# Performance work log

Hardware: AMD Instinct MI355X
Metric: run time of the kernel (lower is better)

## Reference

```python
import jax, jax.numpy as jnp
import numpy as np

K = 8          # knn_graph default k
LOW = 64       # low_res_size
FIRE = 0.5     # fire_rate
HID = 16       # hidden_channels
HEADS = 4      # GAT heads
OUTC = HID // HEADS  # per-head out channels = 4
EPS = 1e-5


def conv3x3(x, W, b):
    y = jax.lax.conv_general_dilated(x, W, (1, 1), 'SAME',
                                     dimension_numbers=('NCHW', 'OIHW', 'NCHW'))
    return y + b[None, :, None, None]


def bnorm(x, g, b, m, v):
    scale = (g / jnp.sqrt(v + EPS))[None, :, None, None]
    return (x - m[None, :, None, None]) * scale + b[None, :, None, None]


def conv1x1(x, W, b):  # W: [out, in]
    return jnp.einsum('bchw,oc->bohw', x, W) + b[None, :, None, None]


def gat_image(nodes, Wg, a_src, a_dst, bg):
    # nodes: [N, HID]. kNN graph (loop=False) + GATConv with self-loops added.
    N = nodes.shape[0]
    sq = jnp.sum(nodes * nodes, axis=1)
    D = sq[:, None] + sq[None, :] - 2.0 * (nodes @ nodes.T)
    D = jax.lax.stop_gradient(D) + jnp.eye(N, dtype=nodes.dtype) * 1e9  # exclude self
    idx = jax.lax.top_k(-D, K)[1]                                   # [N, K] nearest nbrs
    nbr = jnp.concatenate([idx, jnp.arange(N)[:, None]], axis=1)    # [N, K+1] + self-loop
    xp = (nodes @ Wg.T).reshape(N, HEADS, OUTC)                     # [N, H, F]
    asr = jnp.sum(xp * a_src[None], axis=-1)                        # [N, H]
    adt = jnp.sum(xp * a_dst[None], axis=-1)                        # [N, H]
    logits = jax.nn.leaky_relu(asr[nbr] + adt[:, None, :], 0.2)     # [N, K+1, H]
    att = jax.nn.softmax(logits, axis=1)                            # softmax over incoming edges
    out = jnp.sum(att[..., None] * xp[nbr], axis=1)                 # [N, H, F]
    out = out.reshape(N, HEADS * OUTC) + bg
    return jax.nn.relu(out)                                         # GrapherModule relu


def setup_inputs() -> dict:
    key = jax.random.key(0)
    ks = jax.random.split(key, 24)
    f = jnp.float32
    d = {}
    d['x'] = jax.random.normal(ks[0], (8, 1, 256, 256), f)
    d['fire_rand'] = jax.random.uniform(ks[1], (8, 1, LOW, LOW), f)
    # encoder_b1: conv(1->64,3) BN conv(64->16,3) BN
    d['W1'] = jax.random.normal(ks[2], (64, 1, 3, 3), f) * 0.2
    d['b1'] = jax.random.normal(ks[3], (64,), f) * 0.05
    d['g1'] = jnp.ones((64,), f); d['be1'] = jnp.zeros((64,), f)
    d['m1'] = jax.random.normal(ks[4], (64,), f) * 0.1
    d['v1'] = jax.random.uniform(ks[5], (64,), f) + 0.5
    d['W2'] = jax.random.normal(ks[6], (HID, 64, 3, 3), f) * 0.05
    d['b2'] = jax.random.normal(ks[7], (HID,), f) * 0.05
    d['g2'] = jnp.ones((HID,), f); d['be2'] = jnp.zeros((HID,), f)
    d['m2'] = jax.random.normal(ks[8], (HID,), f) * 0.1
    d['v2'] = jax.random.uniform(ks[9], (HID,), f) + 0.5
    # GATConv(16 -> 4 per head, heads=4)
    d['Wg'] = jax.random.normal(ks[10], (HEADS * OUTC, HID), f) * 0.25
    d['a_src'] = jax.random.normal(ks[11], (HEADS, OUTC), f) * 0.5
    d['a_dst'] = jax.random.normal(ks[12], (HEADS, OUTC), f) * 0.5
    d['bg'] = jax.random.normal(ks[13], (HEADS * OUTC,), f) * 0.05
    # update_net_b1: 1x1 conv 16->128->16
    d['Wu1'] = jax.random.normal(ks[14], (128, HID), f) * 0.25
    d['bu1'] = jax.random.normal(ks[15], (128,), f) * 0.05
    d['Wu2'] = jax.random.normal(ks[16], (HID, 128), f) * 0.08
    d['bu2'] = jax.random.normal(ks[17], (HID,), f) * 0.05
    # to_output_b1: 1x1 conv 16->1
    d['Wo'] = jax.random.normal(ks[18], (1, HID), f) * 0.25
    d['bo'] = jax.random.normal(ks[19], (1,), f) * 0.05
    return d


def reference(x, fire_rand, W1, b1, g1, be1, m1, v1, W2, b2, g2, be2, m2, v2,
              Wg, a_src, a_dst, bg, Wu1, bu1, Wu2, bu2, Wo, bo):
    B, C, H, W = x.shape
    xl = jax.image.resize(x, (B, C, LOW, LOW), 'bilinear')
    h = jax.nn.relu(bnorm(conv3x3(xl, W1, b1), g1, be1, m1, v1))
    h = jax.nn.relu(bnorm(conv3x3(h, W2, b2), g2, be2, m2, v2))
    # one NCA step: graph process -> update net -> stochastic fire mask
    N = LOW * LOW
    nodes = h.reshape(B, HID, N).transpose(0, 2, 1)            # [B, N, HID]
    p = jax.vmap(gat_image, in_axes=(0, None, None, None, None))(nodes, Wg, a_src, a_dst, bg)
    p = p.transpose(0, 2, 1).reshape(B, HID, LOW, LOW)
    u = conv1x1(jax.nn.relu(conv1x1(p, Wu1, bu1)), Wu2, bu2)
    mask = (fire_rand < FIRE).astype(h.dtype)                   # [B,1,LOW,LOW]
    h = h + mask * u
    out = jax.nn.sigmoid(conv1x1(h, Wo, bo))
    return jax.image.resize(out, (B, C, H, W), 'bilinear')
```

## Files before the change

### kernel.cpp

```cpp
#include <hip/hip_runtime.h>
#include <math.h>
#include <float.h>

#define BATCH 8
#define HIGH  256
#define LOWR  64
#define NN    4096
#define HIDC  16
#define C1    64
#define NSL   4

#define OFF_XL   0
#define OFF_H1   (OFF_XL  + BATCH*NN)
#define OFF_H    (OFF_H1  + BATCH*C1*NN)
#define OFF_SQ   (OFF_H   + BATCH*NN*HIDC)
#define OFF_XP   (OFF_SQ  + BATCH*NN)
#define OFF_ASR  (OFF_XP  + BATCH*NN*HIDC)
#define OFF_ADT  (OFF_ASR + BATCH*NN*4)
#define OFF_P    (OFF_ADT + BATCH*NN*4)
#define OFF_OL   (OFF_P   + BATCH*NN*HIDC)

typedef __attribute__((ext_vector_type(8)))  short bf16x8;
typedef __attribute__((ext_vector_type(16))) float f32x16;

__device__ __forceinline__ float dot16m(const float ni[16], float4 a0, float4 a1,
                                        float4 a2, float4 a3, float hs) {
    return ni[0]*a0.x + ni[1]*a0.y + ni[2]*a0.z + ni[3]*a0.w
         + ni[4]*a1.x + ni[5]*a1.y + ni[6]*a1.z + ni[7]*a1.w
         + ni[8]*a2.x + ni[9]*a2.y + ni[10]*a2.z + ni[11]*a2.w
         + ni[12]*a3.x + ni[13]*a3.y + ni[14]*a3.z + ni[15]*a3.w
         - hs;
}

__global__ void k_down(const float* __restrict__ x, float* __restrict__ xl) {
    int t = blockIdx.x * 128 + threadIdx.x;
    if (t >= BATCH * NN) return;
    int b = t >> 12, oy = (t >> 6) & 63, ox = t & 63;
    const float* xb = x + b * HIGH * HIGH;
    float cy = 4.f * oy + 1.5f, cx = 4.f * ox + 1.5f;
    float wy[8], wx[8], sy = 0.f, sx = 0.f;
#pragma unroll
    for (int k = 0; k < 8; k++) {
        int iy = 4 * oy - 2 + k;
        float w = 1.f - fabsf((float)iy - cy) * 0.25f;
        if (iy < 0 || iy >= HIGH) w = 0.f;
        wy[k] = w; sy += w;
        int ix = 4 * ox - 2 + k;
        float v = 1.f - fabsf((float)ix - cx) * 0.25f;
        if (ix < 0 || ix >= HIGH) v = 0.f;
        wx[k] = v; sx += v;
    }
    float acc = 0.f;
#pragma unroll
    for (int ky = 0; ky < 8; ky++) {
        if (wy[ky] == 0.f) continue;
        int iy = 4 * oy - 2 + ky;
        float rowacc = 0.f;
#pragma unroll
        for (int kx = 0; kx < 8; kx++) {
            if (wx[kx] == 0.f) continue;
            int ix = 4 * ox - 2 + kx;
            rowacc += wx[kx] * xb[iy * HIGH + ix];
        }
        acc += wy[ky] * rowacc;
    }
    xl[t] = acc / (sy * sx);
}

__global__ void k_conv1(const float* __restrict__ xl, const float* __restrict__ W1,
                        const float* __restrict__ b1, const float* __restrict__ g1,
                        const float* __restrict__ be1, const float* __restrict__ m1,
                        const float* __restrict__ v1, float* __restrict__ h1) {
    int t = blockIdx.x * 256 + threadIdx.x;
    if (t >= BATCH * C1 * NN) return;
    int b = t >> 18, co = (t >> 12) & 63, y = (t >> 6) & 63, x = t & 63;
    const float* src = xl + b * NN;
    const float* w = W1 + co * 9;
    float acc = 0.f;
#pragma unroll
    for (int dy = -1; dy <= 1; dy++) {
        int yy = y + dy; if (yy < 0 || yy >= 64) continue;
#pragma unroll
        for (int dx = -1; dx <= 1; dx++) {
            int xx = x + dx; if (xx < 0 || xx >= 64) continue;
            acc += w[(dy + 1) * 3 + (dx + 1)] * src[yy * 64 + xx];
        }
    }
    acc += b1[co];
    float sc = g1[co] / sqrtf(v1[co] + 1e-5f);
    acc = (acc - m1[co]) * sc + be1[co];
    h1[t] = fmaxf(acc, 0.f);
}

__launch_bounds__(512)
__global__ void k_conv2(const float* __restrict__ h1, const float* __restrict__ W2,
                        const float* __restrict__ b2, const float* __restrict__ g2,
                        const float* __restrict__ be2, const float* __restrict__ m2,
                        const float* __restrict__ v2, const float* __restrict__ Wg,
                        const float* __restrict__ a_src, const float* __restrict__ a_dst,
                        float* __restrict__ h, float* __restrict__ sq,
                        float* __restrict__ xp, float* __restrict__ asr,
                        float* __restrict__ adt) {
    __shared__ float sW2t[576 * 16];
    __shared__ float sWg[256];
    __shared__ float sA[32];
    __shared__ float accH[3][128][17];
    int tid = threadIdx.x;
    for (int k = tid; k < 9216; k += 512) {
        int o = k / 576, ct = k - o * 576;
        sW2t[ct * 16 + o] = W2[k];
    }
    if (tid < 256) sWg[tid] = Wg[tid];
    if (tid < 16) { sA[tid] = a_src[tid]; sA[16 + tid] = a_dst[tid]; }
    __syncthreads();
    int blk = blockIdx.x;
    int b = blk >> 5, ytile = blk & 31;
    int q = tid >> 7;
    int sub = tid & 127;
    int ty = sub >> 6, x = sub & 63, y = ytile * 2 + ty;
    float acc[16];
#pragma unroll
    for (int o = 0; o < 16; o++) acc[o] = 0.f;
    const float* hb = h1 + (long)b * C1 * NN + (long)q * 16 * NN;
    for (int ci = 0; ci < 16; ci++) {
        const float* plane = hb + ci * NN;
#pragma unroll
        for (int dy = -1; dy <= 1; dy++) {
            int yy = y + dy; bool oky = (yy >= 0 && yy < 64);
#pragma unroll
            for (int dx = -1; dx <= 1; dx++) {
                int xx = x + dx;
                float v = (oky && xx >= 0 && xx < 64) ? plane[yy * 64 + xx] : 0.f;
                int ct = (q * 16 + ci) * 9 + (dy + 1) * 3 + (dx + 1);
                const float4* wr = (const float4*)&sW2t[ct * 16];
                float4 w0 = wr[0], w1 = wr[1], w2 = wr[2], w3 = wr[3];
                acc[0] += v * w0.x; acc[1] += v * w0.y; acc[2] += v * w0.z; acc[3] += v * w0.w;
                acc[4] += v * w1.x; acc[5] += v * w1.y; acc[6] += v * w1.z; acc[7] += v * w1.w;
                acc[8] += v * w2.x; acc[9] += v * w2.y; acc[10]+= v * w2.z; acc[11]+= v * w2.w;
                acc[12]+= v * w3.x; acc[13]+= v * w3.y; acc[14]+= v * w3.z; acc[15]+= v * w3.w;
            }
        }
    }
    if (q != 0) {
        float* dst = &accH[q - 1][sub][0];
#pragma unroll
        for (int o = 0; o < 16; o++) dst[o] = acc[o];
    }
    __syncthreads();
    if (q != 0) return;
#pragma unroll
    for (int qq = 0; qq < 3; qq++) {
        const float* src = &accH[qq][sub][0];
#pragma unroll
        for (int o = 0; o < 16; o++) acc[o] += src[o];
    }
    int n = y * 64 + x;
    long node = (long)b * NN + n;
    float nodev[16], sqv = 0.f;
#pragma unroll
    for (int o = 0; o < 16; o++) {
        float a = acc[o] + b2[o];
        float sc = g2[o] / sqrtf(v2[o] + 1e-5f);
        a = (a - m2[o]) * sc + be2[o];
        a = fmaxf(a, 0.f);
        nodev[o] = a; sqv += a * a;
        h[node * 16 + o] = a;
    }
    sq[node] = 0.5f * sqv;
    float xpv[16];
#pragma unroll
    for (int o = 0; o < 16; o++) {
        float a = 0.f;
#pragma unroll
        for (int c = 0; c < 16; c++) a += sWg[o * 16 + c] * nodev[c];
        xpv[o] = a;
        xp[node * 16 + o] = a;
    }
#pragma unroll
    for (int hh = 0; hh < 4; hh++) {
        float as = 0.f, ad = 0.f;
#pragma unroll
        for (int f = 0; f < 4; f++) {
            as += xpv[hh * 4 + f] * sA[hh * 4 + f];
            ad += xpv[hh * 4 + f] * sA[16 + hh * 4 + f];
        }
        asr[node * 4 + hh] = as;
        adt[node * 4 + hh] = ad;
    }
}

__device__ __forceinline__ ushort f2bf(float f) {
    unsigned u = __float_as_uint(f);
    return (ushort)((u + 0x7FFFu + ((u >> 16) & 1u)) >> 16);
}
__device__ __forceinline__ float bf2f(ushort h) {
    return __uint_as_float(((unsigned)h) << 16);
}
__global__ void k_split(const float* __restrict__ h, const float* __restrict__ sq,
                        ushort* __restrict__ hHi, ushort* __restrict__ hMid,
                        ushort* __restrict__ hLo, float* __restrict__ nsq) {
    long t = (long)blockIdx.x * 64 + threadIdx.x;
    nsq[t] = -sq[t];
    const float4* hp = (const float4*)&h[t * 16];
    float4 v0 = hp[0], v1 = hp[1], v2 = hp[2], v3 = hp[3];
    float v[16] = { v0.x,v0.y,v0.z,v0.w, v1.x,v1.y,v1.z,v1.w,
                    v2.x,v2.y,v2.z,v2.w, v3.x,v3.y,v3.z,v3.w };
    unsigned wh[8], wm[8], wl[8];
#pragma unroll
    for (int p = 0; p < 8; p++) {
        unsigned packh = 0, packm = 0, packl = 0;
#pragma unroll
        for (int e = 0; e < 2; e++) {
            float f = v[p * 2 + e];
            ushort hi = f2bf(f);
            float t1 = f - bf2f(hi);
            ushort mi = f2bf(t1);
            float t2 = t1 - bf2f(mi);
            ushort lo = f2bf(t2);
            packh |= ((unsigned)hi) << (16 * e);
            packm |= ((unsigned)mi) << (16 * e);
            packl |= ((unsigned)lo) << (16 * e);
        }
        wh[p] = packh; wm[p] = packm; wl[p] = packl;
    }
    uint4* dh = (uint4*)&hHi[t * 16];
    uint4* dm = (uint4*)&hMid[t * 16];
    uint4* dl = (uint4*)&hLo[t * 16];
    dh[0] = make_uint4(wh[0], wh[1], wh[2], wh[3]);
    dh[1] = make_uint4(wh[4], wh[5], wh[6], wh[7]);
    dm[0] = make_uint4(wm[0], wm[1], wm[2], wm[3]);
    dm[1] = make_uint4(wm[4], wm[5], wm[6], wm[7]);
    dl[0] = make_uint4(wl[0], wl[1], wl[2], wl[3]);
    dl[1] = make_uint4(wl[4], wl[5], wl[6], wl[7]);
}

__device__ __forceinline__ void tile_scores(const ushort* __restrict__ hHi,
        const ushort* __restrict__ hMid, const ushort* __restrict__ hLo,
        const float* __restrict__ nsq, long bN, int j0, int ln31, int koff,
        int rbase, int i0w, bf16x8 bi_h, bf16x8 bi_m, bf16x8 bi_l,
        float scv[16]) {
    int jr = j0 + ln31;
    bf16x8 aj_h = *(const bf16x8*)&hHi [(bN + jr) * 16 + koff];
    bf16x8 aj_m = *(const bf16x8*)&hMid[(bN + jr) * 16 + koff];
    bf16x8 aj_l = *(const bf16x8*)&hLo [(bN + jr) * 16 + koff];
    float4 q0 = *(const float4*)&nsq[bN + j0 +  0 + rbase];
    float4 q1 = *(const float4*)&nsq[bN + j0 +  8 + rbase];
    float4 q2 = *(const float4*)&nsq[bN + j0 + 16 + rbase];
    float4 q3 = *(const float4*)&nsq[bN + j0 + 24 + rbase];
    f32x16 acc;
    acc[0]  = q0.x; acc[1]  = q0.y; acc[2]  = q0.z; acc[3]  = q0.w;
    acc[4]  = q1.x; acc[5]  = q1.y; acc[6]  = q1.z; acc[7]  = q1.w;
    acc[8]  = q2.x; acc[9]  = q2.y; acc[10] = q2.z; acc[11] = q2.w;
    acc[12] = q3.x; acc[13] = q3.y; acc[14] = q3.z; acc[15] = q3.w;
    acc = __builtin_amdgcn_mfma_f32_32x32x16_bf16(aj_h, bi_h, acc, 0, 0, 0);
    acc = __builtin_amdgcn_mfma_f32_32x32x16_bf16(aj_h, bi_m, acc, 0, 0, 0);
    acc = __builtin_amdgcn_mfma_f32_32x32x16_bf16(aj_m, bi_h, acc, 0, 0, 0);
    acc = __builtin_amdgcn_mfma_f32_32x32x16_bf16(aj_h, bi_l, acc, 0, 0, 0);
    acc = __builtin_amdgcn_mfma_f32_32x32x16_bf16(aj_l, bi_h, acc, 0, 0, 0);
    acc = __builtin_amdgcn_mfma_f32_32x32x16_bf16(aj_m, bi_m, acc, 0, 0, 0);
#pragma unroll
    for (int rr = 0; rr < 16; rr++) scv[rr] = acc[rr];
    if (j0 == i0w) {
#pragma unroll
        for (int rr = 0; rr < 16; rr++) {
            int r = (rr & 3) + 8 * (rr >> 2) + rbase;
            if (r == ln31) scv[rr] = -FLT_MAX;
        }
    }
}

#define CEX(a, b) { float ce_hi = fmaxf(a, b), ce_lo = fminf(a, b); (a) = ce_hi; (b) = ce_lo; }
__device__ __forceinline__ void sort8d(float v[8]) {
    CEX(v[0],v[1]); CEX(v[2],v[3]); CEX(v[4],v[5]); CEX(v[6],v[7]);
    CEX(v[0],v[2]); CEX(v[1],v[3]); CEX(v[4],v[6]); CEX(v[5],v[7]);
    CEX(v[1],v[2]); CEX(v[5],v[6]);
    CEX(v[0],v[4]); CEX(v[1],v[5]); CEX(v[2],v[6]); CEX(v[3],v[7]);
    CEX(v[2],v[4]); CEX(v[3],v[5]);
    CEX(v[1],v[2]); CEX(v[3],v[4]); CEX(v[5],v[6]);
}
__device__ __forceinline__ void bsort8d(float v[8]) {
    CEX(v[0],v[4]); CEX(v[1],v[5]); CEX(v[2],v[6]); CEX(v[3],v[7]);
    CEX(v[0],v[2]); CEX(v[1],v[3]); CEX(v[4],v[6]); CEX(v[5],v[7]);
    CEX(v[0],v[1]); CEX(v[2],v[3]); CEX(v[4],v[5]); CEX(v[6],v[7]);
}

__global__ __attribute__((amdgpu_waves_per_eu(4, 4))) __launch_bounds__(256)
void k_scan(const ushort* __restrict__ hHi, const ushort* __restrict__ hMid,
            const ushort* __restrict__ hLo, const float* __restrict__ nsq,
            uint4* __restrict__ cand_i) {
    __shared__ unsigned lists[256][17];
    __shared__ ushort outl[256][8];
    int tid = threadIdx.x, blk = blockIdx.x;
    int b  = blk >> 7;
    int ig = (blk >> 2) & 31;
    int sl = blk & 3;
    int wid = tid >> 6, lane = tid & 63;
    int ln31 = lane & 31, l5 = lane >> 5;
    int koff = l5 * 8;
    int i0w = ig * 128 + wid * 32;
    int i   = i0w + ln31;
    long bN = (long)b * NN;
    int rbase = l5 * 4;
    int jbase = sl * 1024;

    bf16x8 bi_h = *(const bf16x8*)&hHi [(bN + i) * 16 + koff];
    bf16x8 bi_m = *(const bf16x8*)&hMid[(bN + i) * 16 + koff];
    bf16x8 bi_l = *(const bf16x8*)&hLo [(bN + i) * 16 + koff];

    float s[8];
#pragma unroll
    for (int k = 0; k < 8; k++) s[k] = -FLT_MAX;
#pragma unroll 2
    for (int t = 0; t < 32; t++) {
        int j0 = jbase + t * 32;
        float scv[16];
        tile_scores(hHi, hMid, hLo, nsq, bN, j0, ln31, koff, rbase, i0w,
                    bi_h, bi_m, bi_l, scv);
        float va[8] = { scv[0], scv[1], scv[2], scv[3], scv[4], scv[5], scv[6], scv[7] };
        float vb[8] = { scv[8], scv[9], scv[10], scv[11], scv[12], scv[13], scv[14], scv[15] };
        sort8d(va); sort8d(vb);
        float mg[8];
#pragma unroll
        for (int k = 0; k < 8; k++) mg[k] = fmaxf(va[k], vb[7 - k]);
        bsort8d(mg);
#pragma unroll
        for (int k = 0; k < 8; k++) s[k] = fmaxf(s[k], mg[7 - k]);
        bsort8d(s);
    }
    float mv[8];
#pragma unroll
    for (int k = 0; k < 8; k++) mv[k] = fmaxf(s[k], __shfl_xor(s[7 - k], 32));
    float theta = mv[0];
#pragma unroll
    for (int k = 1; k < 8; k++) theta = fminf(theta, mv[k]);

    unsigned* ldsw = &lists[0][0];
    int baseA = tid * 17, baseB = baseA + 8, trash = baseA + 16;
    int nA = 0, nB = 0;
#pragma unroll 2
    for (int t = 0; t < 32; t++) {
        int j0 = jbase + t * 32;
        float scv[16];
        tile_scores(hHi, hMid, hLo, nsq, bN, j0, ln31, koff, rbase, i0w,
                    bi_h, bi_m, bi_l, scv);
        unsigned gm = 0, em = 0;
#pragma unroll
        for (int rr = 0; rr < 16; rr++) {
            gm |= (scv[rr] >  theta) ? (1u << rr) : 0u;
            em |= (scv[rr] == theta) ? (1u << rr) : 0u;
        }
        unsigned m = gm | em;
        while (__any(m != 0u)) {
            if (m) {
                int rr = __ffs(m) - 1;
                m &= m - 1u;
                int r = (rr & 3) + ((rr >> 2) << 3) + rbase;
                int j = j0 + r;
                bool isGt = (gm >> rr) & 1u;
                bool cA = isGt && (nA < 8);
                bool cB = (!isGt) && (nB < 8);
                int ia = cA ? (baseA + nA) : (cB ? (baseB + nB) : trash);
                ldsw[ia] = (unsigned)j;
                nA += cA;
                nB += cB;
            }
        }
    }
    int pA = __shfl_xor(nA, 32);
    int pB = __shfl_xor(nB, 32);
    __syncthreads();
    if (lane < 32) {
        int tp = tid + 32;
        int n = 0;
        for (int k = 0; k < nA && n < 8; k++) outl[tid][n++] = (ushort)lists[tid][k];
        for (int k = 0; k < pA && n < 8; k++) outl[tid][n++] = (ushort)lists[tp][k];
        int p0 = 0, p1 = 0;
        while (n < 8) {
            unsigned a = (p0 < nB) ? lists[tid][8 + p0] : 0xFFFFFFFFu;
            unsigned c = (p1 < pB) ? lists[tp][8 + p1] : 0xFFFFFFFFu;
            bool t0 = a < c;
            outl[tid][n++] = (ushort)(t0 ? a : c);
            p0 += t0 ? 1 : 0; p1 += t0 ? 0 : 1;
        }
        uint4 pk = *(const uint4*)&outl[tid][0];
        cand_i[(long)(b * NSL + sl) * NN + i] = pk;
    }
}

__launch_bounds__(64)
__global__ void k_gat2(const uint4* __restrict__ cand_i, const float* __restrict__ h,
                       const float* __restrict__ sq,
                       const float* __restrict__ xp, const float* __restrict__ asr,
                       const float* __restrict__ adt, const float* __restrict__ bg,
                       float* __restrict__ p) {
    int lane = threadIdx.x;
    int ln31 = lane & 31, half = lane >> 5;
    int t = blockIdx.x * 32 + ln31;
    int b = t >> 12, i = t & 4095;
    long bN = (long)b * NN;
    const float4* ip = (const float4*)&h[(bN + i) * 16];
    float4 r0 = ip[0], r1 = ip[1], r2 = ip[2], r3 = ip[3];
    float ni[16] = { r0.x,r0.y,r0.z,r0.w, r1.x,r1.y,r1.z,r1.w,
                     r2.x,r2.y,r2.z,r2.w, r3.x,r3.y,r3.z,r3.w };
    float fS[8]; int fI[8];
#pragma unroll
    for (int k = 0; k < 8; k++) { fS[k] = -FLT_MAX; fI[k] = 65535; }
#pragma unroll
    for (int ss = 0; ss < 2; ss++) {
        int sl = half * 2 + ss;
        uint4 pk = cand_i[(long)(b * NSL + sl) * NN + i];
        unsigned idx8[8] = { pk.x & 0xFFFF, pk.x >> 16, pk.y & 0xFFFF, pk.y >> 16,
                             pk.z & 0xFFFF, pk.z >> 16, pk.w & 0xFFFF, pk.w >> 16 };
#pragma unroll
        for (int k = 0; k < 8; k++) {
            int j = (int)idx8[k];
            const float4* np = (const float4*)&h[(bN + j) * 16];
            float4 a0 = np[0], a1 = np[1], a2 = np[2], a3 = np[3];
            float d = dot16m(ni, a0, a1, a2, a3, sq[bN + j]);
            bool bt = (d > fS[7]) || (d == fS[7] && j < fI[7]);
            if (bt) {
                fS[7] = d; fI[7] = j;
#pragma unroll
                for (int q = 7; q > 0; q--) {
                    bool sw = (fS[q] > fS[q - 1]) || (fS[q] == fS[q - 1] && fI[q] < fI[q - 1]);
                    if (sw) {
                        float td = fS[q]; fS[q] = fS[q - 1]; fS[q - 1] = td;
                        int tj = fI[q]; fI[q] = fI[q - 1]; fI[q - 1] = tj;
                    }
                }
            }
        }
    }
    float oS[8]; int oI[8];
#pragma unroll
    for (int k = 0; k < 8; k++) {
        oS[k] = __shfl_xor(fS[k], 32);
        oI[k] = __shfl_xor(fI[k], 32);
    }
    int mI[8];
#pragma unroll
    for (int k = 0; k < 8; k++) {
        bool mine = (fS[k] > oS[7 - k]) || (fS[k] == oS[7 - k] && fI[k] < oI[7 - k]);
        mI[k] = mine ? fI[k] : oI[7 - k];
    }
    if (half != 0) return;
    int nbrs[9];
#pragma unroll
    for (int e = 0; e < 8; e++) nbrs[e] = mI[e];
    nbrs[8] = i;
    float adtv[4];
#pragma unroll
    for (int hh = 0; hh < 4; hh++) adtv[hh] = adt[(bN + i) * 4 + hh];
    float mx[4] = { -FLT_MAX, -FLT_MAX, -FLT_MAX, -FLT_MAX };
    float lg[9][4];
#pragma unroll
    for (int e = 0; e < 9; e++) {
        long nb = bN + nbrs[e];
#pragma unroll
        for (int hh = 0; hh < 4; hh++) {
            float l = asr[nb * 4 + hh] + adtv[hh];
            l = (l > 0.f) ? l : 0.2f * l;
            lg[e][hh] = l;
            mx[hh] = fmaxf(mx[hh], l);
        }
    }
    float sum[4] = { 0, 0, 0, 0 };
    float acc[16];
#pragma unroll
    for (int c = 0; c < 16; c++) acc[c] = 0.f;
#pragma unroll
    for (int e = 0; e < 9; e++) {
        long nb = bN + nbrs[e];
        const float4* xpn = (const float4*)&xp[nb * 16];
        float4 x0 = xpn[0], x1 = xpn[1], x2 = xpn[2], x3 = xpn[3];
        float xv[16] = { x0.x,x0.y,x0.z,x0.w, x1.x,x1.y,x1.z,x1.w,
                         x2.x,x2.y,x2.z,x2.w, x3.x,x3.y,x3.z,x3.w };
        float wv[4];
#pragma unroll
        for (int hh = 0; hh < 4; hh++) {
            float w = expf(lg[e][hh] - mx[hh]);
            sum[hh] += w; wv[hh] = w;
        }
#pragma unroll
        for (int hh = 0; hh < 4; hh++)
#pragma unroll
            for (int f = 0; f < 4; f++)
                acc[hh * 4 + f] += wv[hh] * xv[hh * 4 + f];
    }
#pragma unroll
    for (int hh = 0; hh < 4; hh++) {
        float inv = 1.f / sum[hh];
#pragma unroll
        for (int f = 0; f < 4; f++) {
            float o = acc[hh * 4 + f] * inv + bg[hh * 4 + f];
            p[(bN + i) * 16 + hh * 4 + f] = fmaxf(o, 0.f);
        }
    }
}

__launch_bounds__(256)
__global__ void k_update(const float* __restrict__ p, const float* __restrict__ h,
                         const float* __restrict__ fire, const float* __restrict__ Wu1,
                         const float* __restrict__ bu1, const float* __restrict__ Wu2,
                         const float* __restrict__ bu2, const float* __restrict__ Wo,
                         const float* __restrict__ bo, float* __restrict__ out_low) {
    __shared__ float sU1[128 * 16];
    __shared__ float sU2t[128 * 16];
    __shared__ float sb1[128];
    __shared__ float upart[3][64][17];
    int tid = threadIdx.x;
    for (int k = tid; k < 2048; k += 256) {
        sU1[k] = Wu1[k];
        sU2t[(k & 127) * 16 + (k >> 7)] = Wu2[k];
    }
    if (tid < 128) sb1[tid] = bu1[tid];
    __syncthreads();
    int lnode = tid & 63, q = tid >> 6;
    long n = (long)blockIdx.x * 64 + lnode;
    const float4* pp = (const float4*)&p[n * 16];
    float4 p0 = pp[0], p1 = pp[1], p2 = pp[2], p3 = pp[3];
    float pv[16] = { p0.x,p0.y,p0.z,p0.w, p1.x,p1.y,p1.z,p1.w,
                     p2.x,p2.y,p2.z,p2.w, p3.x,p3.y,p3.z,p3.w };
    float u[16];
#pragma unroll
    for (int c = 0; c < 16; c++) u[c] = 0.f;
    int hd0 = q * 32;
    for (int hd = hd0; hd < hd0 + 32; hd++) {
        const float4* r = (const float4*)&sU1[hd * 16];
        float4 r0 = r[0], r1 = r[1], r2 = r[2], r3 = r[3];
        float a = sb1[hd]
            + r0.x*pv[0] + r0.y*pv[1] + r0.z*pv[2] + r0.w*pv[3]
            + r1.x*pv[4] + r1.y*pv[5] + r1.z*pv[6] + r1.w*pv[7]
            + r2.x*pv[8] + r2.y*pv[9] + r2.z*pv[10]+ r2.w*pv[11]
            + r3.x*pv[12]+ r3.y*pv[13]+ r3.z*pv[14]+ r3.w*pv[15];
        a = fmaxf(a, 0.f);
        const float4* tt = (const float4*)&sU2t[hd * 16];
        float4 t0 = tt[0], t1 = tt[1], t2 = tt[2], t3 = tt[3];
        u[0] += t0.x*a; u[1] += t0.y*a; u[2] += t0.z*a; u[3] += t0.w*a;
        u[4] += t1.x*a; u[5] += t1.y*a; u[6] += t1.z*a; u[7] += t1.w*a;
        u[8] += t2.x*a; u[9] += t2.y*a; u[10]+= t2.z*a; u[11]+= t2.w*a;
        u[12]+= t3.x*a; u[13]+= t3.y*a; u[14]+= t3.z*a; u[15]+= t3.w*a;
    }
    if (q != 0) {
        float* dst = &upart[q - 1][lnode][0];
#pragma unroll
        for (int c = 0; c < 16; c++) dst[c] = u[c];
    }
    __syncthreads();
    if (q != 0) return;
#pragma unroll
    for (int qq = 0; qq < 3; qq++) {
        const float* src = &upart[qq][lnode][0];
#pragma unroll
        for (int c = 0; c < 16; c++) u[c] += src[c];
    }
    float mask = (fire[n] < 0.5f) ? 1.f : 0.f;
    const float4* hp = (const float4*)&h[n * 16];
    float4 h0 = hp[0], h1v = hp[1], h2 = hp[2], h3 = hp[3];
    float hv[16] = { h0.x,h0.y,h0.z,h0.w, h1v.x,h1v.y,h1v.z,h1v.w,
                     h2.x,h2.y,h2.z,h2.w, h3.x,h3.y,h3.z,h3.w };
    float o = bo[0];
#pragma unroll
    for (int c = 0; c < 16; c++)
        o += Wo[c] * (hv[c] + mask * (u[c] + bu2[c]));
    out_low[n] = 1.f / (1.f + expf(-o));
}

__global__ void k_up(const float* __restrict__ ol, float* __restrict__ out) {
    int t = blockIdx.x * 256 + threadIdx.x;
    if (t >= BATCH * HIGH * HIGH) return;
    int b = t >> 16, oy = (t >> 8) & 255, ox = t & 255;
    float cy = (oy + 0.5f) * 0.25f - 0.5f;
    float cx = (ox + 0.5f) * 0.25f - 0.5f;
    int iy0 = (int)floorf(cy); float fy = cy - (float)iy0;
    int ix0 = (int)floorf(cx); float fx = cx - (float)ix0;
    int y0 = min(max(iy0, 0), 63), y1 = min(max(iy0 + 1, 0), 63);
    int x0 = min(max(ix0, 0), 63), x1 = min(max(ix0 + 1, 0), 63);
    const float* s = ol + b * NN;
    float v = (1.f - fy) * ((1.f - fx) * s[y0 * 64 + x0] + fx * s[y0 * 64 + x1])
            + fy * ((1.f - fx) * s[y1 * 64 + x0] + fx * s[y1 * 64 + x1]);
    out[t] = v;
}

extern "C" void kernel_launch(void* const* d_in, const int* in_sizes, int n_in,
                              void* d_out, int out_size, void* d_ws, size_t ws_size,
                              hipStream_t stream) {
    const float* x    = (const float*)d_in[0];
    const float* fire = (const float*)d_in[1];
    const float* W1   = (const float*)d_in[2];
    const float* b1   = (const float*)d_in[3];
    const float* g1   = (const float*)d_in[4];
    const float* be1  = (const float*)d_in[5];
    const float* m1   = (const float*)d_in[6];
    const float* v1   = (const float*)d_in[7];
    const float* W2   = (const float*)d_in[8];
    const float* b2   = (const float*)d_in[9];
    const float* g2   = (const float*)d_in[10];
    const float* be2  = (const float*)d_in[11];
    const float* m2   = (const float*)d_in[12];
    const float* v2   = (const float*)d_in[13];
    const float* Wg   = (const float*)d_in[14];
    const float* a_src= (const float*)d_in[15];
    const float* a_dst= (const float*)d_in[16];
    const float* bg   = (const float*)d_in[17];
    const float* Wu1  = (const float*)d_in[18];
    const float* bu1  = (const float*)d_in[19];
    const float* Wu2  = (const float*)d_in[20];
    const float* bu2  = (const float*)d_in[21];
    const float* Wo   = (const float*)d_in[22];
    const float* bo   = (const float*)d_in[23];

    float* ws  = (float*)d_ws;
    float* xl  = ws + OFF_XL;
    float* h1  = ws + OFF_H1;
    float* h   = ws + OFF_H;
    float* sq  = ws + OFF_SQ;
    float* xp  = ws + OFF_XP;
    float* asr = ws + OFF_ASR;
    float* adt = ws + OFF_ADT;
    float* p   = ws + OFF_P;
    float* ol  = ws + OFF_OL;
    uint4*  cand_i = (uint4*)(ws + OFF_H1);
    ushort* hHi    = (ushort*)(ws + OFF_H1 + 1048576);
    ushort* hMid   = (ushort*)(ws + OFF_H1 + 1310720);
    ushort* hLo    = (ushort*)(ws + OFF_H1 + 1572864);
    float*  nsq    = ws + OFF_H1 + 1835008;

    k_down  <<<(BATCH * NN + 127) / 128, 128, 0, stream>>>(x, xl);
    k_conv1 <<<(BATCH * C1 * NN) / 256, 256, 0, stream>>>(xl, W1, b1, g1, be1, m1, v1, h1);
    k_conv2 <<<BATCH * 32, 512, 0, stream>>>(h1, W2, b2, g2, be2, m2, v2, Wg, a_src, a_dst,
                                             h, sq, xp, asr, adt);
    k_split <<<BATCH * NN / 64, 64, 0, stream>>>(h, sq, hHi, hMid, hLo, nsq);
    k_scan  <<<BATCH * 32 * NSL, 256, 0, stream>>>(hHi, hMid, hLo, nsq, cand_i);
    k_gat2  <<<BATCH * NN / 32, 64, 0, stream>>>(cand_i, h, sq, xp, asr, adt, bg, p);
    k_update<<<BATCH * NN / 64, 256, 0, stream>>>(p, h, fire, Wu1, bu1, Wu2, bu2, Wo, bo, ol);
    k_up    <<<(BATCH * HIGH * HIGH) / 256, 256, 0, stream>>>(ol, (float*)d_out);
}
```

Before: 278.7 us.

## Split kNN scan into eight column slices and merge candidates four-way in GAT

The candidate scan now divides each image's columns into eight slices of 512 instead of four of 1024, doubling the number of scan blocks and halving per-block work. The GAT kernel now uses four 16-lane groups per block, each merging two slices. A new index-carrying bitonic sort plus a second shuffle stage merges the four partial top-8 lists. LDS candidate lists shrink to 16-bit entries, and the waves-per-EU hint is relaxed to allow higher occupancy. The cost is more threshold-filtering passes in total, a larger candidate buffer, and a deeper merge in k_gat2.

```diff
diff --git a/kernel.cpp b/kernel.cpp
--- a/kernel.cpp
+++ b/kernel.cpp
@@ -8,7 +8,7 @@
 #define NN    4096
 #define HIDC  16
 #define C1    64
-#define NSL   4
+#define NSL   8
 
 #define OFF_XL   0
 #define OFF_H1   (OFF_XL  + BATCH*NN)
@@ -283,17 +283,30 @@
     CEX(v[0],v[2]); CEX(v[1],v[3]); CEX(v[4],v[6]); CEX(v[5],v[7]);
     CEX(v[0],v[1]); CEX(v[2],v[3]); CEX(v[4],v[5]); CEX(v[6],v[7]);
 }
-
-__global__ __attribute__((amdgpu_waves_per_eu(4, 4))) __launch_bounds__(256)
+#define CEX2(sa, ia, sb, ib) { \
+    bool sw2 = ((sb) > (sa)) || ((sb) == (sa) && (ib) < (ia)); \
+    float th2 = sw2 ? (sb) : (sa); float tl2 = sw2 ? (sa) : (sb); \
+    int   ih2 = sw2 ? (ib) : (ia); int   il2 = sw2 ? (ia) : (ib); \
+    (sa) = th2; (sb) = tl2; (ia) = ih2; (ib) = il2; }
+__device__ __forceinline__ void bsort8d_id(float v[8], int id[8]) {
+    CEX2(v[0],id[0],v[4],id[4]); CEX2(v[1],id[1],v[5],id[5]);
+    CEX2(v[2],id[2],v[6],id[6]); CEX2(v[3],id[3],v[7],id[7]);
+    CEX2(v[0],id[0],v[2],id[2]); CEX2(v[1],id[1],v[3],id[3]);
+    CEX2(v[4],id[4],v[6],id[6]); CEX2(v[5],id[5],v[7],id[7]);
+    CEX2(v[0],id[0],v[1],id[1]); CEX2(v[2],id[2],v[3],id[3]);
+    CEX2(v[4],id[4],v[5],id[5]); CEX2(v[6],id[6],v[7],id[7]);
+}
+
+__global__ __attribute__((amdgpu_waves_per_eu(4, 8))) __launch_bounds__(256)
 void k_scan(const ushort* __restrict__ hHi, const ushort* __restrict__ hMid,
             const ushort* __restrict__ hLo, const float* __restrict__ nsq,
             uint4* __restrict__ cand_i) {
-    __shared__ unsigned lists[256][17];
+    __shared__ ushort lists[256][18];
     __shared__ ushort outl[256][8];
     int tid = threadIdx.x, blk = blockIdx.x;
-    int b  = blk >> 7;
-    int ig = (blk >> 2) & 31;
-    int sl = blk & 3;
+    int b  = blk >> 8;
+    int ig = (blk >> 3) & 31;
+    int sl = blk & 7;
     int wid = tid >> 6, lane = tid & 63;
     int ln31 = lane & 31, l5 = lane >> 5;
     int koff = l5 * 8;
@@ -301,7 +314,7 @@
     int i   = i0w + ln31;
     long bN = (long)b * NN;
     int rbase = l5 * 4;
-    int jbase = sl * 1024;
+    int jbase = sl * 512;
 
     bf16x8 bi_h = *(const bf16x8*)&hHi [(bN + i) * 16 + koff];
     bf16x8 bi_m = *(const bf16x8*)&hMid[(bN + i) * 16 + koff];
@@ -311,7 +324,7 @@
 #pragma unroll
     for (int k = 0; k < 8; k++) s[k] = -FLT_MAX;
 #pragma unroll 2
-    for (int t = 0; t < 32; t++) {
+    for (int t = 0; t < 16; t++) {
         int j0 = jbase + t * 32;
         float scv[16];
         tile_scores(hHi, hMid, hLo, nsq, bN, j0, ln31, koff, rbase, i0w,
@@ -334,11 +347,11 @@
 #pragma unroll
     for (int k = 1; k < 8; k++) theta = fminf(theta, mv[k]);
 
-    unsigned* ldsw = &lists[0][0];
-    int baseA = tid * 17, baseB = baseA + 8, trash = baseA + 16;
+    ushort* ldsw = &lists[0][0];
+    int baseA = tid * 18, baseB = baseA + 8, trash = baseA + 16;
     int nA = 0, nB = 0;
 #pragma unroll 2
-    for (int t = 0; t < 32; t++) {
+    for (int t = 0; t < 16; t++) {
         int j0 = jbase + t * 32;
         float scv[16];
         tile_scores(hHi, hMid, hLo, nsq, bN, j0, ln31, koff, rbase, i0w,
@@ -360,7 +373,7 @@
                 bool cA = isGt && (nA < 8);
                 bool cB = (!isGt) && (nB < 8);
                 int ia = cA ? (baseA + nA) : (cB ? (baseB + nB) : trash);
-                ldsw[ia] = (unsigned)j;
+                ldsw[ia] = (ushort)j;
                 nA += cA;
                 nB += cB;
             }
@@ -372,12 +385,12 @@
     if (lane < 32) {
         int tp = tid + 32;
         int n = 0;
-        for (int k = 0; k < nA && n < 8; k++) outl[tid][n++] = (ushort)lists[tid][k];
-        for (int k = 0; k < pA && n < 8; k++) outl[tid][n++] = (ushort)lists[tp][k];
+        for (int k = 0; k < nA && n < 8; k++) outl[tid][n++] = lists[tid][k];
+        for (int k = 0; k < pA && n < 8; k++) outl[tid][n++] = lists[tp][k];
         int p0 = 0, p1 = 0;
         while (n < 8) {
-            unsigned a = (p0 < nB) ? lists[tid][8 + p0] : 0xFFFFFFFFu;
-            unsigned c = (p1 < pB) ? lists[tp][8 + p1] : 0xFFFFFFFFu;
+            unsigned a = (p0 < nB) ? (unsigned)lists[tid][8 + p0] : 0xFFFFFFFFu;
+            unsigned c = (p1 < pB) ? (unsigned)lists[tp][8 + p1] : 0xFFFFFFFFu;
             bool t0 = a < c;
             outl[tid][n++] = (ushort)(t0 ? a : c);
             p0 += t0 ? 1 : 0; p1 += t0 ? 0 : 1;
@@ -394,8 +407,8 @@
                        const float* __restrict__ adt, const float* __restrict__ bg,
                        float* __restrict__ p) {
     int lane = threadIdx.x;
-    int ln31 = lane & 31, half = lane >> 5;
-    int t = blockIdx.x * 32 + ln31;
+    int ln15 = lane & 15, q = lane >> 4;
+    int t = blockIdx.x * 16 + ln15;
     int b = t >> 12, i = t & 4095;
     long bN = (long)b * NN;
     const float4* ip = (const float4*)&h[(bN + i) * 16];
@@ -407,7 +420,7 @@
     for (int k = 0; k < 8; k++) { fS[k] = -FLT_MAX; fI[k] = 65535; }
 #pragma unroll
     for (int ss = 0; ss < 2; ss++) {
-        int sl = half * 2 + ss;
+        int sl = q * 2 + ss;
         uint4 pk = cand_i[(long)(b * NSL + sl) * NN + i];
         unsigned idx8[8] = { pk.x & 0xFFFF, pk.x >> 16, pk.y & 0xFFFF, pk.y >> 16,
                              pk.z & 0xFFFF, pk.z >> 16, pk.w & 0xFFFF, pk.w >> 16 };
@@ -421,11 +434,11 @@
             if (bt) {
                 fS[7] = d; fI[7] = j;
 #pragma unroll
-                for (int q = 7; q > 0; q--) {
-                    bool sw = (fS[q] > fS[q - 1]) || (fS[q] == fS[q - 1] && fI[q] < fI[q - 1]);
+                for (int qq = 7; qq > 0; qq--) {
+                    bool sw = (fS[qq] > fS[qq - 1]) || (fS[qq] == fS[qq - 1] && fI[qq] < fI[qq - 1]);
                     if (sw) {
-                        float td = fS[q]; fS[q] = fS[q - 1]; fS[q - 1] = td;
-                        int tj = fI[q]; fI[q] = fI[q - 1]; fI[q - 1] = tj;
+                        float td = fS[qq]; fS[qq] = fS[qq - 1]; fS[qq - 1] = td;
+                        int tj = fI[qq]; fI[qq] = fI[qq - 1]; fI[qq - 1] = tj;
                     }
                 }
             }
@@ -434,19 +447,32 @@
     float oS[8]; int oI[8];
 #pragma unroll
     for (int k = 0; k < 8; k++) {
-        oS[k] = __shfl_xor(fS[k], 32);
-        oI[k] = __shfl_xor(fI[k], 32);
-    }
-    int mI[8];
+        oS[k] = __shfl_xor(fS[k], 16);
+        oI[k] = __shfl_xor(fI[k], 16);
+    }
+    float mS[8]; int mI[8];
 #pragma unroll
     for (int k = 0; k < 8; k++) {
         bool mine = (fS[k] > oS[7 - k]) || (fS[k] == oS[7 - k] && fI[k] < oI[7 - k]);
+        mS[k] = mine ? fS[k] : oS[7 - k];
         mI[k] = mine ? fI[k] : oI[7 - k];
     }
-    if (half != 0) return;
+    bsort8d_id(mS, mI);
+#pragma unroll
+    for (int k = 0; k < 8; k++) {
+        oS[k] = __shfl_xor(mS[k], 32);
+        oI[k] = __shfl_xor(mI[k], 32);
+    }
+    int nI[8];
+#pragma unroll
+    for (int k = 0; k < 8; k++) {
+        bool mine = (mS[k] > oS[7 - k]) || (mS[k] == oS[7 - k] && mI[k] < oI[7 - k]);
+        nI[k] = mine ? mI[k] : oI[7 - k];
+    }
+    if (q != 0) return;
     int nbrs[9];
 #pragma unroll
-    for (int e = 0; e < 8; e++) nbrs[e] = mI[e];
+    for (int e = 0; e < 8; e++) nbrs[e] = nI[e];
     nbrs[8] = i;
     float adtv[4];
 #pragma unroll
@@ -632,7 +658,7 @@
                                              h, sq, xp, asr, adt);
     k_split <<<BATCH * NN / 64, 64, 0, stream>>>(h, sq, hHi, hMid, hLo, nsq);
     k_scan  <<<BATCH * 32 * NSL, 256, 0, stream>>>(hHi, hMid, hLo, nsq, cand_i);
-    k_gat2  <<<BATCH * NN / 32, 64, 0, stream>>>(cand_i, h, sq, xp, asr, adt, bg, p);
+    k_gat2  <<<BATCH * NN / 16, 64, 0, stream>>>(cand_i, h, sq, xp, asr, adt, bg, p);
     k_update<<<BATCH * NN / 64, 256, 0, stream>>>(p, h, fire, Wu1, bu1, Wu2, bu2, Wo, bo, ol);
     k_up    <<<(BATCH * HIGH * HIGH) / 256, 256, 0, stream>>>(ol, (float*)d_out);
 }
```

Measured after the change: 277.1 us. No clear change (-0.6%).
